# Kernel optimization log

Hardware: AMD Instinct MI355X
Metric: run time of the kernel (lower is better)

The kernel has to match this reference:

```python
import jax, jax.numpy as jnp
import numpy as np

B, S, D, H = 2, 2048, 1024, 16
DK = D // H
SCALE = DK ** 0.5


def setup_inputs() -> dict:
    key = jax.random.key(0)
    ks = jax.random.split(key, 5)
    std = 1.0 / np.sqrt(D)
    return {
        "x": jax.random.normal(ks[0], (B, S, D), dtype=jnp.float32),
        "Wq": jax.random.normal(ks[1], (D, D), dtype=jnp.float32) * std,
        "Wk": jax.random.normal(ks[2], (D, D), dtype=jnp.float32) * std,
        "Wv": jax.random.normal(ks[3], (D, D), dtype=jnp.float32) * std,
        "Wo": jax.random.normal(ks[4], (D, D), dtype=jnp.float32) * std,
    }


def _split_heads(t):
    # [B, S, D] -> [B, H, S, DK]
    b, s, d = t.shape
    return t.reshape(b, s, H, DK).transpose(0, 2, 1, 3)


def reference(x, Wq, Wk, Wv, Wo):
    b, s, d = x.shape
    q = _split_heads(x @ Wq)
    k = _split_heads(x @ Wk)
    v = _split_heads(x @ Wv)
    # scores: [B, H, S, S]
    score = jnp.einsum("bhqd,bhkd->bhqk", q, k)
    causal = jnp.tril(jnp.ones((s, s), dtype=bool))[None, None]
    score = jnp.where(causal, score, -jnp.inf)
    attn = jax.nn.softmax(score / SCALE, axis=-1)
    out = jnp.einsum("bhqk,bhkd->bhqd", attn, v)
    out = out.transpose(0, 2, 1, 3).reshape(b, s, d)
    return out @ Wo
```

## Files before the change

### kernel.cpp

```cpp
#include <hip/hip_runtime.h>
#include <hip/hip_bf16.h>

typedef __bf16 bf16;
typedef __bf16 bf16x4 __attribute__((ext_vector_type(4)));
typedef __bf16 bf16x8 __attribute__((ext_vector_type(8)));
typedef float f32x4 __attribute__((ext_vector_type(4)));

#define MFMA16(a, b, c) __builtin_amdgcn_mfma_f32_16x16x32_bf16((a), (b), (c), 0, 0, 0)

__device__ __forceinline__ void async16(const void* g, void* l) {
  typedef const unsigned int __attribute__((address_space(1))) * GP;
  typedef unsigned int __attribute__((address_space(3))) * LP;
  __builtin_amdgcn_global_load_lds((GP)g, (LP)l, 16, 0, 0);
}

__global__ __launch_bounds__(256) void prep(
    const float* __restrict__ w0, const float* __restrict__ w1,
    const float* __restrict__ w2, const float* __restrict__ w3,
    const float* __restrict__ x, bf16* __restrict__ wtOut,
    bf16* __restrict__ xOut) {
  const int t = threadIdx.x;
  if (blockIdx.z == 4) {
    size_t base = ((size_t)(blockIdx.y * 16 + blockIdx.x)) * 16384;
#pragma unroll
    for (int p = 0; p < 16; ++p) {
      size_t i = base + (size_t)(p * 256 + t) * 4;
      f32x4 v = *(const f32x4*)&x[i];
      bf16 o[4];
#pragma unroll
      for (int j = 0; j < 4; ++j) o[j] = (bf16)v[j];
      *(ulong1*)&xOut[i] = *(ulong1*)o;
    }
    return;
  }
  __shared__ __align__(16) float tile[64][68];
  const float* src = (blockIdx.z == 0) ? w0 : (blockIdx.z == 1) ? w1
                   : (blockIdx.z == 2) ? w2 : w3;
  bf16* dst = wtOut + (size_t)blockIdx.z * (1024u * 1024u);
  const int bx = blockIdx.x, by = blockIdx.y;
#pragma unroll
  for (int p = 0; p < 4; ++p) {
    int idx = t + p * 256;
    int r = idx >> 4, c4 = idx & 15;
    *(f32x4*)&tile[r][c4 * 4] =
        *(const f32x4*)&src[(size_t)(by * 64 + r) * 1024 + bx * 64 + c4 * 4];
  }
  __syncthreads();
#pragma unroll
  for (int p = 0; p < 2; ++p) {
    int idx = t + p * 256;
    int rn = idx >> 3, c8 = idx & 7;
    bf16x8 v;
#pragma unroll
    for (int i = 0; i < 8; ++i) v[i] = (bf16)tile[c8 * 8 + i][rn];
    *(bf16x8*)&dst[(size_t)(bx * 64 + rn) * 1024 + by * 64 + c8 * 8] = v;
  }
}

template <typename OutT, int NI>
__global__ __launch_bounds__(256, 4) void gemm_bt(
    const bf16* __restrict__ A, const bf16* __restrict__ Bt,
    OutT* __restrict__ C, int btStrideZ, int cStrideZ, float scaleZ0,
    bf16* __restrict__ vtOut) {
  constexpr int XT = 1024 / (NI * 32);
  const int bid = blockIdx.x;
  const int rr = bid & 7, tt = bid >> 3;
  const int xb = tt % XT, yb = (tt / XT) * 8 + rr;
  const int zi = blockIdx.y;

  const int tid = threadIdx.x;
  const int wave = tid >> 6, lane = tid & 63;
  const int quad = lane >> 4, l16 = lane & 15;
  const int wm = wave >> 1, wn = wave & 1;
  const int m0 = yb * 128, n0 = xb * (NI * 32);
  const bf16* Bz = Bt + (size_t)zi * (size_t)btStrideZ;
  OutT* Cz = C + (size_t)zi * (size_t)cStrideZ;
  const float sc = (zi == 0) ? scaleZ0 : 1.0f;

  __shared__ __align__(16) bf16 lsA[2][128 * 32];
  __shared__ __align__(16) bf16 lsB[2][NI * 32 * 32];

  const int lrow = lane >> 2;
  const int cgX = (lane & 3) ^ ((lrow >> 1) & 3);
  const int fR = (l16 >> 1) & 3;

  f32x4 acc[4][NI];
#pragma unroll
  for (int i = 0; i < 4; ++i)
#pragma unroll
    for (int j = 0; j < NI; ++j) acc[i][j] = (f32x4){0.f, 0.f, 0.f, 0.f};

#pragma unroll
  for (int c = 0; c < 2; ++c) {
    int chunk = wave * 2 + c;
    int row = chunk * 16 + lrow;
    async16(&A[(size_t)(m0 + row) * 1024 + cgX * 8], &lsA[0][chunk * 512]);
  }
#pragma unroll
  for (int c = 0; c < NI / 2; ++c) {
    int chunk = wave * (NI / 2) + c;
    int row = chunk * 16 + lrow;
    async16(&Bz[(size_t)(n0 + row) * 1024 + cgX * 8], &lsB[0][chunk * 512]);
  }
  __syncthreads();

  for (int it = 0; it < 32; ++it) {
    const int cur = it & 1;
    if (it < 31) {
      int k0n = (it + 1) * 32;
#pragma unroll
      for (int c = 0; c < 2; ++c) {
        int chunk = wave * 2 + c;
        int row = chunk * 16 + lrow;
        async16(&A[(size_t)(m0 + row) * 1024 + k0n + cgX * 8],
                &lsA[cur ^ 1][chunk * 512]);
      }
#pragma unroll
      for (int c = 0; c < NI / 2; ++c) {
        int chunk = wave * (NI / 2) + c;
        int row = chunk * 16 + lrow;
        async16(&Bz[(size_t)(n0 + row) * 1024 + k0n + cgX * 8],
                &lsB[cur ^ 1][chunk * 512]);
      }
    }

    bf16x8 af[4], bfr[NI];
#pragma unroll
    for (int i = 0; i < 4; ++i) {
      int ra = wm * 64 + i * 16 + l16;
      af[i] = *(const bf16x8*)&lsA[cur][ra * 32 + ((quad ^ fR) * 8)];
    }
#pragma unroll
    for (int ni = 0; ni < NI; ++ni) {
      int rb = wn * (NI * 16) + ni * 16 + l16;
      bfr[ni] = *(const bf16x8*)&lsB[cur][rb * 32 + ((quad ^ fR) * 8)];
    }
#pragma unroll
    for (int mi = 0; mi < 4; ++mi)
#pragma unroll
      for (int ni = 0; ni < NI; ++ni)
        acc[mi][ni] = MFMA16(af[mi], bfr[ni], acc[mi][ni]);

    __syncthreads();
  }

  if (zi == 2 && vtOut != nullptr) {
#pragma unroll
    for (int mi = 0; mi < 4; ++mi)
#pragma unroll
      for (int ni = 0; ni < NI; ++ni) {
        int col = n0 + wn * (NI * 16) + ni * 16 + l16;
        int hd = col >> 6, d = col & 63;
        int row = m0 + wm * 64 + mi * 16 + quad * 4;
        int b = row >> 11, s = row & 2047;
        int s32 = s & 31;
        int sp = (s & ~31) + ((s32 & 12) << 1) + ((s32 >> 4) << 2);
        bf16 o[4];
#pragma unroll
        for (int r = 0; r < 4; ++r) o[r] = (bf16)acc[mi][ni][r];
        *(ulong1*)&vtOut[((size_t)(b * 16 + hd) * 64 + d) * 2048 + sp] =
            *(ulong1*)o;
      }
  } else {
#pragma unroll
    for (int mi = 0; mi < 4; ++mi)
#pragma unroll
      for (int ni = 0; ni < NI; ++ni) {
        int col = n0 + wn * (NI * 16) + ni * 16 + l16;
#pragma unroll
        for (int r = 0; r < 4; ++r) {
          int row = m0 + wm * 64 + mi * 16 + quad * 4 + r;
          Cz[(size_t)row * 1024 + col] = (OutT)(acc[mi][ni][r] * sc);
        }
      }
  }
}

__global__ __launch_bounds__(256, 4) void attn_fwd(
    const bf16* __restrict__ Q, const bf16* __restrict__ K,
    const bf16* __restrict__ Vt, bf16* __restrict__ O) {
  const int bid = blockIdx.x;
  const int xcd = bid & 7;
  const int i = bid >> 3;
  const int g4 = i & 3;
  const int j = i >> 2;
  const int a = j & 7, bq = j >> 3;
  const int qt = (bq < 2) ? (31 - 2 * a - bq) : (2 * a + (bq & 1));
  const int bh = xcd * 4 + g4;
  const int h = bh & 15, b = bh >> 4;
  const int tid = threadIdx.x;
  const int wave = tid >> 6, lane = tid & 63;
  const int quad = lane >> 4, l16 = lane & 15;
  const int qh = wave >> 1;
  const int kh = wave & 1;

  __shared__ __align__(16) bf16 SMEM[20480];
  bf16* Qs = &SMEM[16384];

  const size_t base = ((size_t)b * 2048) * 1024 + (size_t)h * 64;
  const bf16* Qb = Q + base;
  const bf16* Kb = K + base;
  const bf16* Vtb = Vt + ((size_t)(b * 16 + h)) * 64 * 2048;
  bf16* Ob = O + base;

  const int lrow = lane >> 3;
  const int cgX = (lane & 7) ^ lrow;

#pragma unroll
  for (int c = 0; c < 2; ++c) {
    int chunk = wave * 2 + c;
    int row = chunk * 8 + lrow;
    async16(&Qb[(size_t)(qt * 64 + row) * 1024 + cgX * 8], &Qs[chunk * 512]);
    async16(&Kb[(size_t)row * 1024 + cgX * 8], &SMEM[chunk * 512]);
    async16(&Vtb[(size_t)row * 2048 + cgX * 8], &SMEM[4096 + chunk * 512]);
  }
  __syncthreads();

  bf16x8 aq[2][2];
#pragma unroll
  for (int g = 0; g < 2; ++g)
#pragma unroll
    for (int ks = 0; ks < 2; ++ks) {
      int row = qh * 32 + g * 16 + l16;
      aq[g][ks] =
          *(const bf16x8*)&Qs[row * 64 + (((ks * 4 + quad) ^ (l16 & 7)) * 8)];
    }

  const float NEG_INF = -__builtin_inff();
  f32x4 lsv[2];
  f32x4 Oacc[2][4];
#pragma unroll
  for (int g = 0; g < 2; ++g) {
    lsv[g] = (f32x4){0.f, 0.f, 0.f, 0.f};
#pragma unroll
    for (int nt = 0; nt < 4; ++nt) Oacc[g][nt] = (f32x4){0.f, 0.f, 0.f, 0.f};
  }

  for (int kt = 0; kt <= qt; ++kt) {
    const int cur = kt & 1;
    if (kt < qt) {
      const int ns = (cur ^ 1) * 8192;
#pragma unroll
      for (int c = 0; c < 2; ++c) {
        int chunk = wave * 2 + c;
        int row = chunk * 8 + lrow;
        async16(&Kb[(size_t)((kt + 1) * 64 + row) * 1024 + cgX * 8],
                &SMEM[ns + chunk * 512]);
        async16(&Vtb[(size_t)row * 2048 + (kt + 1) * 64 + cgX * 8],
                &SMEM[ns + 4096 + chunk * 512]);
      }
    }

    const int ko = cur * 8192;
    const int vo = ko + 4096;
    const bool diag = (kt == qt);

    if (!(diag && kh == 1 && qh == 0)) {
      f32x4 s[2][2];
#pragma unroll
      for (int t = 0; t < 2; ++t) {
        const int row = kh * 32 + t * 16 + l16;
        bf16x8 bk0 =
            *(const bf16x8*)&SMEM[ko + row * 64 + ((quad ^ (l16 & 7)) * 8)];
        bf16x8 bk1 = *(const bf16x8*)&SMEM[ko + row * 64 +
                                           (((4 + quad) ^ (l16 & 7)) * 8)];
        __builtin_amdgcn_s_setprio(1);
#pragma unroll
        for (int g = 0; g < 2; ++g) {
          f32x4 sv = (f32x4){0.f, 0.f, 0.f, 0.f};
          sv = MFMA16(bk0, aq[g][0], sv);
          sv = MFMA16(bk1, aq[g][1], sv);
          s[g][t] = sv;
        }
        __builtin_amdgcn_s_setprio(0);
      }

      if (diag) {
#pragma unroll
        for (int g = 0; g < 2; ++g) {
          const int q_rel = qh * 32 + g * 16 + l16;
#pragma unroll
          for (int t = 0; t < 2; ++t) {
            const int kb = kh * 32 + t * 16 + quad * 4;
#pragma unroll
            for (int r = 0; r < 4; ++r)
              if (kb + r > q_rel) s[g][t][r] = NEG_INF;
          }
        }
      }

      bf16x8 apf[2];
#pragma unroll
      for (int g = 0; g < 2; ++g) {
#pragma unroll
        for (int t = 0; t < 2; ++t) {
#pragma unroll
          for (int r = 0; r < 4; ++r)
            s[g][t][r] = __builtin_amdgcn_exp2f(s[g][t][r]);
          lsv[g] += s[g][t];
        }
        bf16x4 c0 = __builtin_convertvector(s[g][0], bf16x4);
        bf16x4 c1 = __builtin_convertvector(s[g][1], bf16x4);
#pragma unroll
        for (int i2 = 0; i2 < 4; ++i2) {
          apf[g][i2] = c0[i2];
          apf[g][4 + i2] = c1[i2];
        }
      }

#pragma unroll
      for (int nt = 0; nt < 4; ++nt) {
        const int R = nt * 16 + l16;
        bf16x8 bvf = *(const bf16x8*)&SMEM[vo + R * 64 +
                                           (((kh * 4 + quad) ^ (l16 & 7)) *
                                            8)];
        __builtin_amdgcn_s_setprio(1);
#pragma unroll
        for (int g = 0; g < 2; ++g)
          Oacc[g][nt] = MFMA16(apf[g], bvf, Oacc[g][nt]);
        __builtin_amdgcn_s_setprio(0);
      }
    }

    __syncthreads();
  }

  float* F = (float*)SMEM;
  const int qoff = qh * 2560;
  if (kh == 1) {
#pragma unroll
    for (int g = 0; g < 2; ++g) {
#pragma unroll
      for (int nt = 0; nt < 4; ++nt)
        *(f32x4*)&F[qoff + (g * 4 + nt) * 256 + lane * 4] = Oacc[g][nt];
      *(f32x4*)&F[qoff + 2048 + g * 256 + lane * 4] = lsv[g];
    }
  }
  __syncthreads();
  if (kh == 0) {
#pragma unroll
    for (int g = 0; g < 2; ++g) {
#pragma unroll
      for (int nt = 0; nt < 4; ++nt)
        Oacc[g][nt] += *(const f32x4*)&F[qoff + (g * 4 + nt) * 256 + lane * 4];
      lsv[g] += *(const f32x4*)&F[qoff + 2048 + g * 256 + lane * 4];
    }
    float ls[2];
#pragma unroll
    for (int g = 0; g < 2; ++g) {
      float a_ = lsv[g][0] + lsv[g][1] + lsv[g][2] + lsv[g][3];
      a_ += __shfl_xor(a_, 16, 64);
      a_ += __shfl_xor(a_, 32, 64);
      ls[g] = a_;
    }
    float rl[2][4];
#pragma unroll
    for (int g = 0; g < 2; ++g)
#pragma unroll
      for (int r = 0; r < 4; ++r)
        rl[g][r] = 1.f / __shfl(ls[g], quad * 4 + r, 64);
#pragma unroll
    for (int g = 0; g < 2; ++g)
#pragma unroll
      for (int nt = 0; nt < 4; ++nt)
#pragma unroll
        for (int r = 0; r < 4; ++r) {
          int row = qt * 64 + qh * 32 + g * 16 + quad * 4 + r;
          Ob[(size_t)row * 1024 + nt * 16 + l16] =
              (bf16)(Oacc[g][nt][r] * rl[g][r]);
        }
  }
}

extern "C" void kernel_launch(void* const* d_in, const int* in_sizes, int n_in,
                              void* d_out, int out_size, void* d_ws,
                              size_t ws_size, hipStream_t stream) {
  (void)in_sizes; (void)n_in; (void)out_size; (void)ws_size;
  const float* x  = (const float*)d_in[0];
  const float* Wq = (const float*)d_in[1];
  const float* Wk = (const float*)d_in[2];
  const float* Wv = (const float*)d_in[3];
  const float* Wo = (const float*)d_in[4];
  float* out = (float*)d_out;

  bf16* ws = (bf16*)d_ws;
  const size_t WELEM = 1024u * 1024u;
  const size_t TELEM = 4096u * 1024u;
  bf16* wt  = ws;
  bf16* xbf = ws + 4 * WELEM;
  bf16* q   = xbf + TELEM;
  bf16* k   = q + TELEM;
  bf16* vt  = k + TELEM;
  bf16* ao  = vt + TELEM;

  const float QSCALE = 0.125f * 1.44269504088896340736f;

  prep<<<dim3(16, 16, 5), 256, 0, stream>>>(Wq, Wk, Wv, Wo, x, wt, xbf);
  gemm_bt<bf16, 4><<<dim3(256, 3), 256, 0, stream>>>(
      xbf, wt, q, (int)WELEM, (int)TELEM, QSCALE, vt);
  attn_fwd<<<dim3(1024), 256, 0, stream>>>(q, k, vt, ao);
  gemm_bt<float, 2><<<dim3(512, 1), 256, 0, stream>>>(
      ao, wt + 3 * WELEM, out, 0, 0, 1.0f, nullptr);
}
```

Baseline: 160.0 us.

## Split long causal query tiles across two blocks and combine partial results

The 16 longest query tiles per head are each split into two blocks that cover halves of the key range, so the attention grid grows to 1536 blocks with more even per-block work. Each split block writes unnormalized fp32 partial outputs and row sums to workspace, and a new combine kernel adds them and normalizes. This targets load imbalance from the causal triangle, at the cost of extra global traffic, an extra launch, and reliance on the softmax having no running max subtraction so partials can simply be summed.

```diff
diff --git a/kernel.cpp b/kernel.cpp
--- a/kernel.cpp
+++ b/kernel.cpp
@@ -178,14 +178,28 @@
 
 __global__ __launch_bounds__(256, 4) void attn_fwd(
     const bf16* __restrict__ Q, const bf16* __restrict__ K,
-    const bf16* __restrict__ Vt, bf16* __restrict__ O) {
+    const bf16* __restrict__ Vt, bf16* __restrict__ O,
+    float* __restrict__ Pout) {
   const int bid = blockIdx.x;
   const int xcd = bid & 7;
   const int i = bid >> 3;
   const int g4 = i & 3;
   const int j = i >> 2;
-  const int a = j & 7, bq = j >> 3;
-  const int qt = (bq < 2) ? (31 - 2 * a - bq) : (2 * a + (bq & 1));
+  int qt, kt0, ktend, half = 0;
+  bool split;
+  if (j < 32) {
+    qt = 31 - (j >> 1);
+    half = j & 1;
+    const int nt2 = (qt + 1) >> 1;
+    split = true;
+    kt0 = half ? nt2 : 0;
+    ktend = half ? (qt + 1) : nt2;
+  } else {
+    qt = 47 - j;
+    split = false;
+    kt0 = 0;
+    ktend = qt + 1;
+  }
   const int bh = xcd * 4 + g4;
   const int h = bh & 15, b = bh >> 4;
   const int tid = threadIdx.x;
@@ -206,13 +220,16 @@
   const int lrow = lane >> 3;
   const int cgX = (lane & 7) ^ lrow;
 
+  const int s0 = (kt0 & 1) * 8192;
 #pragma unroll
   for (int c = 0; c < 2; ++c) {
     int chunk = wave * 2 + c;
     int row = chunk * 8 + lrow;
     async16(&Qb[(size_t)(qt * 64 + row) * 1024 + cgX * 8], &Qs[chunk * 512]);
-    async16(&Kb[(size_t)row * 1024 + cgX * 8], &SMEM[chunk * 512]);
-    async16(&Vtb[(size_t)row * 2048 + cgX * 8], &SMEM[4096 + chunk * 512]);
+    async16(&Kb[(size_t)(kt0 * 64 + row) * 1024 + cgX * 8],
+            &SMEM[s0 + chunk * 512]);
+    async16(&Vtb[(size_t)row * 2048 + kt0 * 64 + cgX * 8],
+            &SMEM[s0 + 4096 + chunk * 512]);
   }
   __syncthreads();
 
@@ -236,9 +253,9 @@
     for (int nt = 0; nt < 4; ++nt) Oacc[g][nt] = (f32x4){0.f, 0.f, 0.f, 0.f};
   }
 
-  for (int kt = 0; kt <= qt; ++kt) {
+  for (int kt = kt0; kt < ktend; ++kt) {
     const int cur = kt & 1;
-    if (kt < qt) {
+    if (kt + 1 < ktend) {
       const int ns = (cur ^ 1) * 8192;
 #pragma unroll
       for (int c = 0; c < 2; ++c) {
@@ -353,23 +370,62 @@
       a_ += __shfl_xor(a_, 32, 64);
       ls[g] = a_;
     }
-    float rl[2][4];
-#pragma unroll
-    for (int g = 0; g < 2; ++g)
-#pragma unroll
-      for (int r = 0; r < 4; ++r)
-        rl[g][r] = 1.f / __shfl(ls[g], quad * 4 + r, 64);
-#pragma unroll
-    for (int g = 0; g < 2; ++g)
-#pragma unroll
-      for (int nt = 0; nt < 4; ++nt)
-#pragma unroll
-        for (int r = 0; r < 4; ++r) {
-          int row = qt * 64 + qh * 32 + g * 16 + quad * 4 + r;
-          Ob[(size_t)row * 1024 + nt * 16 + l16] =
-              (bf16)(Oacc[g][nt][r] * rl[g][r]);
-        }
-  }
+    if (!split) {
+      float rl[2][4];
+#pragma unroll
+      for (int g = 0; g < 2; ++g)
+#pragma unroll
+        for (int r = 0; r < 4; ++r)
+          rl[g][r] = 1.f / __shfl(ls[g], quad * 4 + r, 64);
+#pragma unroll
+      for (int g = 0; g < 2; ++g)
+#pragma unroll
+        for (int nt = 0; nt < 4; ++nt)
+#pragma unroll
+          for (int r = 0; r < 4; ++r) {
+            int row = qt * 64 + qh * 32 + g * 16 + quad * 4 + r;
+            Ob[(size_t)row * 1024 + nt * 16 + l16] =
+                (bf16)(Oacc[g][nt][r] * rl[g][r]);
+          }
+    } else {
+      float* P = Pout + ((size_t)(bh * 32 + qt) * 2 + half) * 4160;
+#pragma unroll
+      for (int g = 0; g < 2; ++g) {
+#pragma unroll
+        for (int nt = 0; nt < 4; ++nt)
+#pragma unroll
+          for (int r = 0; r < 4; ++r) {
+            int row = qh * 32 + g * 16 + quad * 4 + r;
+            P[row * 64 + nt * 16 + l16] = Oacc[g][nt][r];
+          }
+        if (quad == 0) P[4096 + qh * 32 + g * 16 + l16] = ls[g];
+      }
+    }
+  }
+}
+
+__global__ __launch_bounds__(256) void attn_combine(
+    const float* __restrict__ P, bf16* __restrict__ O) {
+  const int bh = blockIdx.x >> 4;
+  const int qt = 16 + (blockIdx.x & 15);
+  const int h = bh & 15, b = bh >> 4;
+  const float* P0 = P + ((size_t)(bh * 32 + qt) * 2) * 4160;
+  const float* P1 = P0 + 4160;
+  const int t = threadIdx.x;
+  const int row = t >> 2, c0 = (t & 3) * 16;
+  const float rl = 1.f / (P0[4096 + row] + P1[4096 + row]);
+  bf16* Ob =
+      O + ((size_t)b * 2048 + qt * 64 + row) * 1024 + h * 64 + c0;
+  bf16 o[16];
+#pragma unroll
+  for (int i = 0; i < 16; i += 4) {
+    f32x4 a = *(const f32x4*)&P0[row * 64 + c0 + i];
+    f32x4 bb = *(const f32x4*)&P1[row * 64 + c0 + i];
+#pragma unroll
+    for (int r = 0; r < 4; ++r) o[i + r] = (bf16)((a[r] + bb[r]) * rl);
+  }
+#pragma unroll
+  for (int i = 0; i < 16; i += 4) *(ulong1*)&Ob[i] = *(ulong1*)&o[i];
 }
 
 extern "C" void kernel_launch(void* const* d_in, const int* in_sizes, int n_in,
@@ -392,13 +448,15 @@
   bf16* k   = q + TELEM;
   bf16* vt  = k + TELEM;
   bf16* ao  = vt + TELEM;
+  float* pO = (float*)(ao + TELEM);
 
   const float QSCALE = 0.125f * 1.44269504088896340736f;
 
   prep<<<dim3(16, 16, 5), 256, 0, stream>>>(Wq, Wk, Wv, Wo, x, wt, xbf);
   gemm_bt<bf16, 4><<<dim3(256, 3), 256, 0, stream>>>(
       xbf, wt, q, (int)WELEM, (int)TELEM, QSCALE, vt);
-  attn_fwd<<<dim3(1024), 256, 0, stream>>>(q, k, vt, ao);
+  attn_fwd<<<dim3(1536), 256, 0, stream>>>(q, k, vt, ao, pO);
+  attn_combine<<<dim3(512), 256, 0, stream>>>(pO, ao);
   gemm_bt<float, 2><<<dim3(512, 1), 256, 0, stream>>>(
       ao, wt + 3 * WELEM, out, 0, 0, 1.0f, nullptr);
 }
```

Measured after the change: 172.4 us. 1.08x slower.
